# Performance work log

Hardware: AMD Instinct MI355X
Metric: run time of the kernel (lower is better)

Reference implementation:

```python
import jax, jax.numpy as jnp
import numpy as np

B, S, D = 4, 2048, 1024
E, H, TOPK = 8, 4096, 2


def setup_inputs() -> dict:
    key = jax.random.key(0)
    ks = jax.random.split(key, 6)
    scale_d = 1.0 / np.sqrt(D)
    scale_h = 1.0 / np.sqrt(H)
    return {
        "x": jax.random.normal(ks[0], (B, S, D), dtype=jnp.float32),
        "gate_w": jax.random.normal(ks[1], (D, E), dtype=jnp.float32) * scale_d,
        "w1": jax.random.normal(ks[2], (E, D, H), dtype=jnp.float32) * scale_d,
        "b1": jnp.zeros((E, H), dtype=jnp.float32),
        "w2": jax.random.normal(ks[3], (E, H, D), dtype=jnp.float32) * scale_h,
        "b2": jnp.zeros((E, D), dtype=jnp.float32),
    }


def reference(x, gate_w, w1, b1, w2, b2):
    # Gate: logits [B, S, E], top-k routing, softmax over the k selected logits
    gate_logits = jnp.einsum("bsd,de->bse", x, gate_w)
    topw, sel = jax.lax.top_k(gate_logits, TOPK)          # [B, S, K]
    topw = jax.nn.softmax(topw.astype(jnp.float32), axis=-1).astype(x.dtype)

    out = jnp.zeros_like(x)
    # Loop over the small, fixed expert set (structurally distinct params).
    for i in range(E):
        # combine weight for expert i per token (0 if not routed to i)
        coef = jnp.sum(jnp.where(sel == i, topw, jnp.zeros((), x.dtype)), axis=-1)  # [B, S]
        h = jax.nn.gelu(jnp.einsum("bsd,dh->bsh", x, w1[i]) + b1[i])
        y = jnp.einsum("bsh,hd->bsd", h, w2[i]) + b2[i]
        out = out + coef[..., None] * y
    return out
```

## Files before the change

kernel.cpp:

```cpp
#include <hip/hip_runtime.h>
#include <hip/hip_bf16.h>

#define T_TOKENS 8192
#define D_DIM 1024
#define H_DIM 4096
#define E_NUM 8
#define CAP 8192
#define CNT_PAD 16

#define TPB_G 32
#define GATE_BLKS (T_TOKENS / TPB_G)
#define TRW1_BLKS ((D_DIM / 64) * (H_DIM / 64) * E_NUM)
#define TRW2_BLKS ((H_DIM / 64) * (D_DIM / 64) * E_NUM)

typedef short bf16x8 __attribute__((ext_vector_type(8)));
typedef float f32x4 __attribute__((ext_vector_type(4)));
typedef unsigned short u16x8 __attribute__((ext_vector_type(8)));

__device__ inline unsigned short f2bf(float f) {
    __hip_bfloat16 h = __float2bfloat16(f);
    return *reinterpret_cast<unsigned short*>(&h);
}

__device__ inline float gelu_sig(float v) {
    float x = v * (1.5957691216057308f + 0.07135481627f * v * v);
    return v * __builtin_amdgcn_rcpf(1.0f + __expf(-x));
}

__device__ inline void gld_lds16(const unsigned short* g, unsigned short* lds) {
    __builtin_amdgcn_global_load_lds(
        (const __attribute__((address_space(1))) void*)g,
        (__attribute__((address_space(3))) void*)lds, 16, 0, 0);
}

#define WAITV(N) do { asm volatile("s_waitcnt vmcnt(" #N ")" ::: "memory"); \
                      __builtin_amdgcn_sched_barrier(0); } while (0)
#define LGKM0    do { asm volatile("s_waitcnt lgkmcnt(0)" ::: "memory"); \
                      __builtin_amdgcn_sched_barrier(0); } while (0)
#define SBAR     do { __builtin_amdgcn_sched_barrier(0); \
                      __builtin_amdgcn_s_barrier(); \
                      __builtin_amdgcn_sched_barrier(0); } while (0)

#define XCD_ITEMS(T)                                                          \
    int xcd = blockIdx.x & 7;                                                 \
    int lb  = blockIdx.x >> 3;                                                \
    int nbx = gridDim.x >> 3;                                                 \
    int q_ = (T) >> 3, r_ = (T) & 7;                                          \
    int base_ = (xcd < r_) ? xcd * (q_ + 1) : r_ * (q_ + 1) + (xcd - r_) * q_;\
    int cntx_ = (xcd < r_) ? q_ + 1 : q_;

__device__ inline void trw_body(const float* __restrict__ w,
                                unsigned short* __restrict__ wt,
                                int K, int N, int bb,
                                unsigned short (*tb)[72]) {
    int nk = K / 64, nn = N / 64;
    int e = bb / (nk * nn);
    int rem = bb - e * (nk * nn);
    int k0 = (rem % nk) * 64;
    int n0 = (rem / nk) * 64;
    const float* we = w + (size_t)e * K * N + (size_t)k0 * N + n0;
    unsigned short* wte = wt + (size_t)e * K * N + (size_t)n0 * K + k0;
    int tid = threadIdx.x;

    int kg = tid >> 4;
    int nq = (tid & 15) * 4;
    float4 r0 = *(const float4*)(we + (size_t)(kg * 4 + 0) * N + nq);
    float4 r1 = *(const float4*)(we + (size_t)(kg * 4 + 1) * N + nq);
    float4 r2 = *(const float4*)(we + (size_t)(kg * 4 + 2) * N + nq);
    float4 r3 = *(const float4*)(we + (size_t)(kg * 4 + 3) * N + nq);
    ushort4 u;
    u.x = f2bf(r0.x); u.y = f2bf(r1.x); u.z = f2bf(r2.x); u.w = f2bf(r3.x);
    *(ushort4*)&tb[nq + 0][kg * 4] = u;
    u.x = f2bf(r0.y); u.y = f2bf(r1.y); u.z = f2bf(r2.y); u.w = f2bf(r3.y);
    *(ushort4*)&tb[nq + 1][kg * 4] = u;
    u.x = f2bf(r0.z); u.y = f2bf(r1.z); u.z = f2bf(r2.z); u.w = f2bf(r3.z);
    *(ushort4*)&tb[nq + 2][kg * 4] = u;
    u.x = f2bf(r0.w); u.y = f2bf(r1.w); u.z = f2bf(r2.w); u.w = f2bf(r3.w);
    *(ushort4*)&tb[nq + 3][kg * 4] = u;

    __syncthreads();

#pragma unroll
    for (int p = 0; p < 2; ++p) {
        int n = p * 32 + (tid >> 3);
        int kc = (tid & 7) * 8;
        u16x8 v = *(const u16x8*)&tb[n][kc];
        *(u16x8*)(wte + (size_t)n * K + kc) = v;
    }
}

__global__ __launch_bounds__(256) void prep_kernel(const float* __restrict__ x,
                                                   const float* __restrict__ gw,
                                                   const float* __restrict__ w1,
                                                   const float* __restrict__ w2,
                                                   int* __restrict__ cnt,
                                                   int* __restrict__ tok,
                                                   float* __restrict__ cf,
                                                   unsigned short* __restrict__ xb,
                                                   unsigned short* __restrict__ w1t,
                                                   unsigned short* __restrict__ w2t) {
    __shared__ __align__(16) unsigned short tb[64][72];
    __shared__ int ls0[TPB_G], ls1[TPB_G];
    __shared__ float lp0[TPB_G], lp1[TPB_G];
    int b = blockIdx.x;
    if (b >= GATE_BLKS) {
        int bb = b - GATE_BLKS;
        if (bb < TRW1_BLKS) trw_body(w1, w1t, D_DIM, H_DIM, bb, tb);
        else                trw_body(w2, w2t, H_DIM, D_DIM, bb - TRW1_BLKS, tb);
        return;
    }
    int tid = threadIdx.x;
    int lane = tid & 63, wv = tid >> 6;
#pragma unroll
    for (int rep = 0; rep < TPB_G / 4; ++rep) {
        int ti = rep * 4 + wv;
        int t = b * TPB_G + ti;
        const float* xr = x + (size_t)t * D_DIM;
        unsigned short* xbr = xb + (size_t)t * D_DIM;
        double acc[E_NUM];
#pragma unroll
        for (int e = 0; e < E_NUM; ++e) acc[e] = 0.0;
#pragma unroll
        for (int it = 0; it < 4; ++it) {
            int d = it * 256 + lane * 4;
            float4 v = *(const float4*)(xr + d);
            ushort4 u;
            u.x = f2bf(v.x); u.y = f2bf(v.y); u.z = f2bf(v.z); u.w = f2bf(v.w);
            *(ushort4*)(xbr + d) = u;
            const float vv[4] = {v.x, v.y, v.z, v.w};
#pragma unroll
            for (int j = 0; j < 4; ++j) {
                const float* g = gw + (size_t)(d + j) * E_NUM;
#pragma unroll
                for (int e = 0; e < E_NUM; ++e) acc[e] += (double)vv[j] * (double)g[e];
            }
        }
#pragma unroll
        for (int e = 0; e < E_NUM; ++e) {
            double v = acc[e];
#pragma unroll
            for (int off = 32; off >= 1; off >>= 1) v += __shfl_xor(v, off);
            acc[e] = v;
        }
        if (lane == 0) {
            int s0 = 0;
#pragma unroll
            for (int e = 1; e < E_NUM; ++e) if (acc[e] > acc[s0]) s0 = e;
            int s1 = -1;
#pragma unroll
            for (int e = 0; e < E_NUM; ++e) if (e != s0 && (s1 < 0 || acc[e] > acc[s1])) s1 = e;
            float l0 = (float)acc[s0], l1 = (float)acc[s1];
            float p1 = __expf(l1 - l0);
            float inv = 1.0f / (1.0f + p1);
            ls0[ti] = s0; ls1[ti] = s1;
            lp0[ti] = inv; lp1[ti] = p1 * inv;
        }
    }
    __syncthreads();
    if (tid < E_NUM) {
        int e = tid, c = 0;
#pragma unroll
        for (int i = 0; i < TPB_G; ++i) c += (ls0[i] == e) + (ls1[i] == e);
        if (c > 0) {
            int q = atomicAdd(&cnt[e * CNT_PAD], c);
            for (int i = 0; i < TPB_G; ++i) {
                int t = b * TPB_G + i;
                if (ls0[i] == e) { tok[e * CAP + q] = t; cf[e * CAP + q] = lp0[i]; ++q; }
                if (ls1[i] == e) { tok[e * CAP + q] = t; cf[e * CAP + q] = lp1[i]; ++q; }
            }
        }
    }
}


__global__ __launch_bounds__(512, 2) void gemm1_fast(const unsigned short* __restrict__ xb,
                                                     const unsigned short* __restrict__ w1t,
                                                     const float* __restrict__ b1,
                                                     const int* __restrict__ cnt,
                                                     const int* __restrict__ tok,
                                                     unsigned short* __restrict__ Hbuf) {
    __shared__ __align__(16) unsigned short As[3][256][32];
    __shared__ __align__(16) unsigned short Bs[3][256][32];
    __shared__ int s_tok[256];

    int tid = threadIdx.x, lane = tid & 63, wv = tid >> 6;
    int wm = wv >> 2, wn = wv & 3;
    int lm = lane & 15, lkq = lane >> 4;
    int srow = tid >> 2;
    int schunk = (((tid & 3) ^ (srow & 3)) << 3);
    int rdc = ((lkq ^ (lm & 3)) << 3);

    int ne_[E_NUM], offs_[E_NUM], pref[E_NUM + 1];
    pref[0] = 0;
    int off = 0;
#pragma unroll
    for (int e = 0; e < E_NUM; ++e) {
        ne_[e] = cnt[e * CNT_PAD];
        offs_[e] = off; off += ne_[e];
        pref[e + 1] = pref[e] + ((ne_[e] + 255) >> 8) * 16;
    }
    int T = pref[E_NUM];

    XCD_ITEMS(T)
    for (int ii = lb; ii < cntx_; ii += nbx) {
        int w = base_ + ii;
        int e = 0;
#pragma unroll
        for (int q = 0; q < E_NUM - 1; ++q) e += (w >= pref[q + 1]) ? 1 : 0;
        int local = w - pref[e];
        int bm0 = (local >> 4) * 256;
        int n0 = (local & 15) * 256;
        int ne = ne_[e];
        int offs = offs_[e];
        const unsigned short* w1e = w1t + (size_t)e * H_DIM * D_DIM;

        __syncthreads();
        if (tid < 256) s_tok[tid] = tok[e * CAP + min(bm0 + tid, ne - 1)];
        __syncthreads();

        const unsigned short* gA[2];
        const unsigned short* gB[2];
#pragma unroll
        for (int u = 0; u < 2; ++u) {
            gA[u] = xb + (size_t)s_tok[u * 128 + srow] * D_DIM + schunk;
            gB[u] = w1e + (size_t)(n0 + u * 128 + srow) * D_DIM + schunk;
        }
        float bias_v[4];
#pragma unroll
        for (int j = 0; j < 4; ++j)
            bias_v[j] = b1[(size_t)e * H_DIM + n0 + wn * 64 + j * 16 + lm];

        f32x4 acc[8][4];
#pragma unroll
        for (int i = 0; i < 8; ++i)
#pragma unroll
            for (int j = 0; j < 4; ++j) { f32x4 z = {0.f, 0.f, 0.f, 0.f}; acc[i][j] = z; }

        auto STAGE_A = [&](int sl, int kb, int u) {
            gld_lds16(gA[u] + kb * 32, &As[sl][u * 128 + wv * 16][0]);
        };
        auto STAGE_B = [&](int sl, int kb, int u) {
            gld_lds16(gB[u] + kb * 32, &Bs[sl][u * 128 + wv * 16][0]);
        };

        const int NT = D_DIM / 32;
        STAGE_A(0, 0, 0); STAGE_A(0, 0, 1); STAGE_B(0, 0, 0); STAGE_B(0, 0, 1);
        STAGE_A(1, 1, 0); STAGE_A(1, 1, 1); STAGE_B(1, 1, 0); STAGE_B(1, 1, 1);

        int s = 0, s2 = 2;
        for (int t = 0; t < NT; ++t) {
            if (t + 1 < NT) { WAITV(4); } else { WAITV(0); }
            SBAR;
            bf16x8 bfr[4], afr[4];
#pragma unroll
            for (int f = 0; f < 4; ++f)
                bfr[f] = *(const bf16x8*)&Bs[s][wn * 64 + f * 16 + lm][rdc];
#pragma unroll
            for (int f = 0; f < 4; ++f)
                afr[f] = *(const bf16x8*)&As[s][wm * 128 + f * 16 + lm][rdc];
            if (t + 2 < NT) { STAGE_A(s2, t + 2, 0); STAGE_A(s2, t + 2, 1); }
            LGKM0;
            __builtin_amdgcn_s_setprio(1);
#pragma unroll
            for (int i = 0; i < 4; ++i)
#pragma unroll
                for (int j = 0; j < 4; ++j)
                    acc[i][j] = __builtin_amdgcn_mfma_f32_16x16x32_bf16(afr[i], bfr[j], acc[i][j], 0, 0, 0);
            __builtin_amdgcn_s_setprio(0);
#pragma unroll
            for (int f = 0; f < 4; ++f)
                afr[f] = *(const bf16x8*)&As[s][wm * 128 + 64 + f * 16 + lm][rdc];
            if (t + 2 < NT) { STAGE_B(s2, t + 2, 0); STAGE_B(s2, t + 2, 1); }
            LGKM0;
            __builtin_amdgcn_s_setprio(1);
#pragma unroll
            for (int i = 0; i < 4; ++i)
#pragma unroll
                for (int j = 0; j < 4; ++j)
                    acc[4 + i][j] = __builtin_amdgcn_mfma_f32_16x16x32_bf16(afr[i], bfr[j], acc[4 + i][j], 0, 0, 0);
            __builtin_amdgcn_s_setprio(0);
            s = (s == 2) ? 0 : s + 1;
            s2 = (s2 == 2) ? 0 : s2 + 1;
        }

#pragma unroll
        for (int i = 0; i < 8; ++i) {
            int frow = wm * 128 + ((i < 4) ? i * 16 : 64 + (i - 4) * 16);
#pragma unroll
            for (int r = 0; r < 4; ++r) {
                int row = frow + lkq * 4 + r;
                int gr = bm0 + row;
                if (gr >= ne) continue;
                size_t rb = (size_t)(offs + gr) * H_DIM;
#pragma unroll
                for (int j = 0; j < 4; ++j) {
                    int gn = n0 + wn * 64 + j * 16 + lm;
                    float v = acc[i][j][r] + bias_v[j];
                    Hbuf[rb + gn] = f2bf(gelu_sig(v));
                }
            }
        }
    }
}

__global__ __launch_bounds__(512, 2) void gemm2_fast(const unsigned short* __restrict__ Hbuf,
                                                     const unsigned short* __restrict__ w2t,
                                                     const float* __restrict__ b2,
                                                     const int* __restrict__ cnt,
                                                     const int* __restrict__ tok,
                                                     const float* __restrict__ cf,
                                                     float* __restrict__ out) {
    __shared__ __align__(16) unsigned short As[3][256][32];
    __shared__ __align__(16) unsigned short Bs[3][256][32];
    __shared__ int s_tok[256];
    __shared__ float s_cf[256];

    int tid = threadIdx.x, lane = tid & 63, wv = tid >> 6;
    int wm = wv >> 2, wn = wv & 3;
    int lm = lane & 15, lkq = lane >> 4;
    int srow = tid >> 2;
    int schunk = (((tid & 3) ^ (srow & 3)) << 3);
    int rdc = ((lkq ^ (lm & 3)) << 3);

    int ne_[E_NUM], offs_[E_NUM], pref[E_NUM + 1];
    pref[0] = 0;
    int off = 0;
#pragma unroll
    for (int e = 0; e < E_NUM; ++e) {
        ne_[e] = cnt[e * CNT_PAD];
        offs_[e] = off; off += ne_[e];
        pref[e + 1] = pref[e] + ((ne_[e] + 255) >> 8) * 4;
    }
    int T = pref[E_NUM];

    XCD_ITEMS(T)
    for (int ii = lb; ii < cntx_; ii += nbx) {
        int w = base_ + ii;
        int e = 0;
#pragma unroll
        for (int q = 0; q < E_NUM - 1; ++q) e += (w >= pref[q + 1]) ? 1 : 0;
        int local = w - pref[e];
        int bm0 = (local >> 2) * 256;
        int n0 = (local & 3) * 256;
        int ne = ne_[e];
        int offs = offs_[e];
        const unsigned short* w2e = w2t + (size_t)e * H_DIM * D_DIM;

        __syncthreads();
        if (tid < 256) {
            int gi = min(bm0 + tid, ne - 1);
            s_tok[tid] = tok[e * CAP + gi];
            s_cf[tid] = cf[e * CAP + gi];
        }
        __syncthreads();

        const unsigned short* gA[2];
        const unsigned short* gB[2];
#pragma unroll
        for (int u = 0; u < 2; ++u) {
            gA[u] = Hbuf + (size_t)(offs + min(bm0 + u * 128 + srow, ne - 1)) * H_DIM + schunk;
            gB[u] = w2e + (size_t)(n0 + u * 128 + srow) * H_DIM + schunk;
        }
        float bias_v[4];
#pragma unroll
        for (int j = 0; j < 4; ++j)
            bias_v[j] = b2[(size_t)e * D_DIM + n0 + wn * 64 + j * 16 + lm];

        f32x4 acc[8][4];
#pragma unroll
        for (int i = 0; i < 8; ++i)
#pragma unroll
            for (int j = 0; j < 4; ++j) { f32x4 z = {0.f, 0.f, 0.f, 0.f}; acc[i][j] = z; }

        auto STAGE_A = [&](int sl, int kb, int u) {
            gld_lds16(gA[u] + kb * 32, &As[sl][u * 128 + wv * 16][0]);
        };
        auto STAGE_B = [&](int sl, int kb, int u) {
            gld_lds16(gB[u] + kb * 32, &Bs[sl][u * 128 + wv * 16][0]);
        };

        const int NT = H_DIM / 32;
        STAGE_A(0, 0, 0); STAGE_A(0, 0, 1); STAGE_B(0, 0, 0); STAGE_B(0, 0, 1);
        STAGE_A(1, 1, 0); STAGE_A(1, 1, 1); STAGE_B(1, 1, 0); STAGE_B(1, 1, 1);

        int s = 0, s2 = 2;
        for (int t = 0; t < NT; ++t) {
            if (t + 1 < NT) { WAITV(4); } else { WAITV(0); }
            SBAR;
            bf16x8 bfr[4], afr[4];
#pragma unroll
            for (int f = 0; f < 4; ++f)
                bfr[f] = *(const bf16x8*)&Bs[s][wn * 64 + f * 16 + lm][rdc];
#pragma unroll
            for (int f = 0; f < 4; ++f)
                afr[f] = *(const bf16x8*)&As[s][wm * 128 + f * 16 + lm][rdc];
            if (t + 2 < NT) { STAGE_A(s2, t + 2, 0); STAGE_A(s2, t + 2, 1); }
            LGKM0;
            __builtin_amdgcn_s_setprio(1);
#pragma unroll
            for (int i = 0; i < 4; ++i)
#pragma unroll
                for (int j = 0; j < 4; ++j)
                    acc[i][j] = __builtin_amdgcn_mfma_f32_16x16x32_bf16(afr[i], bfr[j], acc[i][j], 0, 0, 0);
            __builtin_amdgcn_s_setprio(0);
#pragma unroll
            for (int f = 0; f < 4; ++f)
                afr[f] = *(const bf16x8*)&As[s][wm * 128 + 64 + f * 16 + lm][rdc];
            if (t + 2 < NT) { STAGE_B(s2, t + 2, 0); STAGE_B(s2, t + 2, 1); }
            LGKM0;
            __builtin_amdgcn_s_setprio(1);
#pragma unroll
            for (int i = 0; i < 4; ++i)
#pragma unroll
                for (int j = 0; j < 4; ++j)
                    acc[4 + i][j] = __builtin_amdgcn_mfma_f32_16x16x32_bf16(afr[i], bfr[j], acc[4 + i][j], 0, 0, 0);
            __builtin_amdgcn_s_setprio(0);
            s = (s == 2) ? 0 : s + 1;
            s2 = (s2 == 2) ? 0 : s2 + 1;
        }

#pragma unroll
        for (int i = 0; i < 8; ++i) {
            int frow = wm * 128 + ((i < 4) ? i * 16 : 64 + (i - 4) * 16);
#pragma unroll
            for (int r = 0; r < 4; ++r) {
                int row = frow + lkq * 4 + r;
                int gr = bm0 + row;
                if (gr >= ne) continue;
                int tk = s_tok[row];
                float cw = s_cf[row];
#pragma unroll
                for (int j = 0; j < 4; ++j) {
                    int gn = n0 + wn * 64 + j * 16 + lm;
                    float y = acc[i][j][r] + bias_v[j];
                    atomicAdd(&out[(size_t)tk * D_DIM + gn], cw * y);
                }
            }
        }
    }
}

extern "C" void kernel_launch(void* const* d_in, const int* in_sizes, int n_in,
                              void* d_out, int out_size, void* d_ws, size_t ws_size,
                              hipStream_t stream) {
    const float* x  = (const float*)d_in[0];
    const float* gw = (const float*)d_in[1];
    const float* w1 = (const float*)d_in[2];
    const float* b1 = (const float*)d_in[3];
    const float* w2 = (const float*)d_in[4];
    const float* b2 = (const float*)d_in[5];
    float* out = (float*)d_out;

    char* ws = (char*)d_ws;
    const size_t SZ_CNT   = E_NUM * CNT_PAD * 4;
    const size_t SZ_ROUTE = SZ_CNT + (size_t)2 * E_NUM * CAP * 4;
    const size_t SZ_XB    = (size_t)T_TOKENS * D_DIM * 2;
    const size_t SZ_W     = (size_t)E_NUM * D_DIM * H_DIM * 2;
    const size_t SZ_H     = (size_t)2 * T_TOKENS * H_DIM * 2;

    int*   cnt = (int*)ws;
    int*   tok = (int*)(ws + SZ_CNT);
    float* cff = (float*)(ws + SZ_CNT + E_NUM * CAP * 4);

    size_t need_fast = SZ_ROUTE + SZ_XB + 2 * SZ_W + SZ_H;
    if (ws_size < need_fast) return;

    unsigned short* xb   = (unsigned short*)(ws + SZ_ROUTE);
    unsigned short* w1t  = (unsigned short*)(ws + SZ_ROUTE + SZ_XB);
    unsigned short* w2t  = (unsigned short*)(ws + SZ_ROUTE + SZ_XB + SZ_W);
    unsigned short* Hbuf = (unsigned short*)(ws + SZ_ROUTE + SZ_XB + 2 * SZ_W);

    hipMemsetAsync(cnt, 0, SZ_CNT, stream);
    hipMemsetAsync(out, 0, (size_t)out_size * sizeof(float), stream);

    prep_kernel<<<GATE_BLKS + TRW1_BLKS + TRW2_BLKS, 256, 0, stream>>>(
        x, gw, w1, w2, cnt, tok, cff, xb, w1t, w2t);

    gemm1_fast<<<256, 512, 0, stream>>>(xb, w1t, b1, cnt, tok, Hbuf);
    gemm2_fast<<<256, 512, 0, stream>>>(Hbuf, w2t, b2, cnt, tok, cff, out);
}
```

Baseline: 614.1 us.

## Restructure MoE GEMM mainloops to BK=64 ping-pong with quarter-step staging

Both expert GEMM kernels move from a three-stage BK=32 LDS ring to two BK=64 ping-pong buffers. Each K step is split into four quadrant phases that interleave fragment loads, async global-to-LDS staging of the next tile, and MFMA bursts, separated by barriers. The XOR swizzle widens to 8 chunks and launch bounds drop to one block per CU to fit the larger LDS footprint. The aim is fewer barriers per unit of MFMA work and better load/compute overlap, at the cost of occupancy and more barriers inside each step.

```diff
diff --git a/kernel.cpp b/kernel.cpp
--- a/kernel.cpp
+++ b/kernel.cpp
@@ -33,13 +33,13 @@
         (__attribute__((address_space(3))) void*)lds, 16, 0, 0);
 }
 
-#define WAITV(N) do { asm volatile("s_waitcnt vmcnt(" #N ")" ::: "memory"); \
-                      __builtin_amdgcn_sched_barrier(0); } while (0)
-#define LGKM0    do { asm volatile("s_waitcnt lgkmcnt(0)" ::: "memory"); \
-                      __builtin_amdgcn_sched_barrier(0); } while (0)
-#define SBAR     do { __builtin_amdgcn_sched_barrier(0); \
-                      __builtin_amdgcn_s_barrier(); \
-                      __builtin_amdgcn_sched_barrier(0); } while (0)
+#define WAITV0 do { asm volatile("s_waitcnt vmcnt(0)" ::: "memory"); \
+                    __builtin_amdgcn_sched_barrier(0); } while (0)
+#define LGKM0  do { asm volatile("s_waitcnt lgkmcnt(0)" ::: "memory"); \
+                    __builtin_amdgcn_sched_barrier(0); } while (0)
+#define SBAR   do { __builtin_amdgcn_sched_barrier(0); \
+                    __builtin_amdgcn_s_barrier(); \
+                    __builtin_amdgcn_sched_barrier(0); } while (0)
 
 #define XCD_ITEMS(T)                                                          \
     int xcd = blockIdx.x & 7;                                                 \
@@ -173,22 +173,45 @@
 }
 
 
-__global__ __launch_bounds__(512, 2) void gemm1_fast(const unsigned short* __restrict__ xb,
+#define GEMM_CORE(AR, BR, AW, BW, tcur, last)                                 \
+    WAITV0; SBAR;                                                             \
+                                                     \
+    LDA4(AR, 0); LDB2(BR, 0);                                                 \
+    if (!(last)) { STG_A(AW, (tcur) + 1, 0); STG_B(BW, (tcur) + 1, 0); }      \
+    LGKM0; MMQ(0, 0);                                                         \
+    SBAR;                                                                     \
+                                                     \
+    LDB2(BR, 1);                                                              \
+    if (!(last)) { STG_A(AW, (tcur) + 1, 1); STG_B(BW, (tcur) + 1, 1); }      \
+    LGKM0; MMQ(0, 1);                                                         \
+    SBAR;                                                                     \
+                                     \
+    LDA4(AR, 1);                                                              \
+    if (!(last)) { STG_A(AW, (tcur) + 1, 2); STG_B(BW, (tcur) + 1, 2); }      \
+    LGKM0; MMQ(1, 1);                                                         \
+    SBAR;                                                                     \
+                                                     \
+    LDB2(BR, 0);                                                              \
+    if (!(last)) { STG_A(AW, (tcur) + 1, 3); STG_B(BW, (tcur) + 1, 3); }      \
+    LGKM0; MMQ(1, 0);
+
+__global__ __launch_bounds__(512, 1) void gemm1_fast(const unsigned short* __restrict__ xb,
                                                      const unsigned short* __restrict__ w1t,
                                                      const float* __restrict__ b1,
                                                      const int* __restrict__ cnt,
                                                      const int* __restrict__ tok,
                                                      unsigned short* __restrict__ Hbuf) {
-    __shared__ __align__(16) unsigned short As[3][256][32];
-    __shared__ __align__(16) unsigned short Bs[3][256][32];
+    __shared__ __align__(16) unsigned short As0[256][64], Bs0[256][64];
+    __shared__ __align__(16) unsigned short As1[256][64], Bs1[256][64];
     __shared__ int s_tok[256];
 
     int tid = threadIdx.x, lane = tid & 63, wv = tid >> 6;
     int wm = wv >> 2, wn = wv & 3;
     int lm = lane & 15, lkq = lane >> 4;
-    int srow = tid >> 2;
-    int schunk = (((tid & 3) ^ (srow & 3)) << 3);
-    int rdc = ((lkq ^ (lm & 3)) << 3);
+    int srow = tid >> 3;
+    int schunk = ((tid & 7) ^ (srow & 7)) << 3;
+    int rdc0 = ((lkq ^ (lm & 7)) << 3);
+    int rdc1 = (((4 + lkq) ^ (lm & 7)) << 3);
 
     int ne_[E_NUM], offs_[E_NUM], pref[E_NUM + 1];
     pref[0] = 0;
@@ -218,13 +241,12 @@
         if (tid < 256) s_tok[tid] = tok[e * CAP + min(bm0 + tid, ne - 1)];
         __syncthreads();
 
-        const unsigned short* gA[2];
-        const unsigned short* gB[2];
-#pragma unroll
-        for (int u = 0; u < 2; ++u) {
-            gA[u] = xb + (size_t)s_tok[u * 128 + srow] * D_DIM + schunk;
-            gB[u] = w1e + (size_t)(n0 + u * 128 + srow) * D_DIM + schunk;
-        }
+        const unsigned short* gA[4];
+#pragma unroll
+        for (int q = 0; q < 4; ++q)
+            gA[q] = xb + (size_t)s_tok[q * 64 + srow] * D_DIM + schunk;
+        const unsigned short* gB = w1e + (size_t)(n0 + srow) * D_DIM + schunk;
+
         float bias_v[4];
 #pragma unroll
         for (int j = 0; j < 4; ++j)
@@ -236,59 +258,59 @@
 #pragma unroll
             for (int j = 0; j < 4; ++j) { f32x4 z = {0.f, 0.f, 0.f, 0.f}; acc[i][j] = z; }
 
-        auto STAGE_A = [&](int sl, int kb, int u) {
-            gld_lds16(gA[u] + kb * 32, &As[sl][u * 128 + wv * 16][0]);
+        bf16x8 afr[4][2], bfr[2][2];
+
+        auto STG_A = [&](unsigned short (&A)[256][64], int kb, int q) {
+            gld_lds16(gA[q] + kb * 64, &A[q * 64 + wv * 8][0]);
         };
-        auto STAGE_B = [&](int sl, int kb, int u) {
-            gld_lds16(gB[u] + kb * 32, &Bs[sl][u * 128 + wv * 16][0]);
+        auto STG_B = [&](unsigned short (&B)[256][64], int kb, int q) {
+            gld_lds16(gB + (size_t)(q * 64) * D_DIM + kb * 64, &B[q * 64 + wv * 8][0]);
         };
-
-        const int NT = D_DIM / 32;
-        STAGE_A(0, 0, 0); STAGE_A(0, 0, 1); STAGE_B(0, 0, 0); STAGE_B(0, 0, 1);
-        STAGE_A(1, 1, 0); STAGE_A(1, 1, 1); STAGE_B(1, 1, 0); STAGE_B(1, 1, 1);
-
-        int s = 0, s2 = 2;
-        for (int t = 0; t < NT; ++t) {
-            if (t + 1 < NT) { WAITV(4); } else { WAITV(0); }
-            SBAR;
-            bf16x8 bfr[4], afr[4];
-#pragma unroll
-            for (int f = 0; f < 4; ++f)
-                bfr[f] = *(const bf16x8*)&Bs[s][wn * 64 + f * 16 + lm][rdc];
-#pragma unroll
-            for (int f = 0; f < 4; ++f)
-                afr[f] = *(const bf16x8*)&As[s][wm * 128 + f * 16 + lm][rdc];
-            if (t + 2 < NT) { STAGE_A(s2, t + 2, 0); STAGE_A(s2, t + 2, 1); }
-            LGKM0;
-            __builtin_amdgcn_s_setprio(1);
-#pragma unroll
-            for (int i = 0; i < 4; ++i)
-#pragma unroll
-                for (int j = 0; j < 4; ++j)
-                    acc[i][j] = __builtin_amdgcn_mfma_f32_16x16x32_bf16(afr[i], bfr[j], acc[i][j], 0, 0, 0);
-            __builtin_amdgcn_s_setprio(0);
-#pragma unroll
-            for (int f = 0; f < 4; ++f)
-                afr[f] = *(const bf16x8*)&As[s][wm * 128 + 64 + f * 16 + lm][rdc];
-            if (t + 2 < NT) { STAGE_B(s2, t + 2, 0); STAGE_B(s2, t + 2, 1); }
-            LGKM0;
-            __builtin_amdgcn_s_setprio(1);
-#pragma unroll
-            for (int i = 0; i < 4; ++i)
-#pragma unroll
-                for (int j = 0; j < 4; ++j)
-                    acc[4 + i][j] = __builtin_amdgcn_mfma_f32_16x16x32_bf16(afr[i], bfr[j], acc[4 + i][j], 0, 0, 0);
-            __builtin_amdgcn_s_setprio(0);
-            s = (s == 2) ? 0 : s + 1;
-            s2 = (s2 == 2) ? 0 : s2 + 1;
-        }
+#define LDA4(AR, mh)                                                          \
+        _Pragma("unroll")                                                     \
+        for (int f = 0; f < 4; ++f) {                                         \
+            int row = wm * 128 + ((mh) * 4 + f) * 16 + lm;                    \
+            afr[f][0] = *(const bf16x8*)&AR[row][rdc0];                       \
+            afr[f][1] = *(const bf16x8*)&AR[row][rdc1];                       \
+        }
+#define LDB2(BR, nh)                                                          \
+        _Pragma("unroll")                                                     \
+        for (int j = 0; j < 2; ++j) {                                         \
+            int col = wn * 64 + ((nh) * 2 + j) * 16 + lm;                     \
+            bfr[j][0] = *(const bf16x8*)&BR[col][rdc0];                       \
+            bfr[j][1] = *(const bf16x8*)&BR[col][rdc1];                       \
+        }
+#define MMQ(mh, nh)                                                           \
+        __builtin_amdgcn_s_setprio(1);                                        \
+        _Pragma("unroll")                                                     \
+        for (int f = 0; f < 4; ++f)                                           \
+            _Pragma("unroll")                                                 \
+            for (int j = 0; j < 2; ++j) {                                     \
+                acc[(mh) * 4 + f][(nh) * 2 + j] =                             \
+                    __builtin_amdgcn_mfma_f32_16x16x32_bf16(                  \
+                        afr[f][0], bfr[j][0], acc[(mh) * 4 + f][(nh) * 2 + j], 0, 0, 0); \
+                acc[(mh) * 4 + f][(nh) * 2 + j] =                             \
+                    __builtin_amdgcn_mfma_f32_16x16x32_bf16(                  \
+                        afr[f][1], bfr[j][1], acc[(mh) * 4 + f][(nh) * 2 + j], 0, 0, 0); \
+            }                                                                 \
+        __builtin_amdgcn_s_setprio(0);
+
+        const int NT = D_DIM / 64;
+#pragma unroll
+        for (int q = 0; q < 4; ++q) { STG_A(As0, 0, q); STG_B(Bs0, 0, q); }
+        for (int t = 0; t < NT; t += 2) {
+            GEMM_CORE(As0, Bs0, As1, Bs1, t, false)
+            GEMM_CORE(As1, Bs1, As0, Bs0, t + 1, (t + 2 >= NT))
+        }
+#undef LDA4
+#undef LDB2
+#undef MMQ
 
 #pragma unroll
         for (int i = 0; i < 8; ++i) {
-            int frow = wm * 128 + ((i < 4) ? i * 16 : 64 + (i - 4) * 16);
 #pragma unroll
             for (int r = 0; r < 4; ++r) {
-                int row = frow + lkq * 4 + r;
+                int row = wm * 128 + i * 16 + lkq * 4 + r;
                 int gr = bm0 + row;
                 if (gr >= ne) continue;
                 size_t rb = (size_t)(offs + gr) * H_DIM;
@@ -303,24 +325,25 @@
     }
 }
 
-__global__ __launch_bounds__(512, 2) void gemm2_fast(const unsigned short* __restrict__ Hbuf,
+__global__ __launch_bounds__(512, 1) void gemm2_fast(const unsigned short* __restrict__ Hbuf,
                                                      const unsigned short* __restrict__ w2t,
                                                      const float* __restrict__ b2,
                                                      const int* __restrict__ cnt,
                                                      const int* __restrict__ tok,
                                                      const float* __restrict__ cf,
                                                      float* __restrict__ out) {
-    __shared__ __align__(16) unsigned short As[3][256][32];
-    __shared__ __align__(16) unsigned short Bs[3][256][32];
+    __shared__ __align__(16) unsigned short As0[256][64], Bs0[256][64];
+    __shared__ __align__(16) unsigned short As1[256][64], Bs1[256][64];
     __shared__ int s_tok[256];
     __shared__ float s_cf[256];
 
     int tid = threadIdx.x, lane = tid & 63, wv = tid >> 6;
     int wm = wv >> 2, wn = wv & 3;
     int lm = lane & 15, lkq = lane >> 4;
-    int srow = tid >> 2;
-    int schunk = (((tid & 3) ^ (srow & 3)) << 3);
-    int rdc = ((lkq ^ (lm & 3)) << 3);
+    int srow = tid >> 3;
+    int schunk = ((tid & 7) ^ (srow & 7)) << 3;
+    int rdc0 = ((lkq ^ (lm & 7)) << 3);
+    int rdc1 = (((4 + lkq) ^ (lm & 7)) << 3);
 
     int ne_[E_NUM], offs_[E_NUM], pref[E_NUM + 1];
     pref[0] = 0;
@@ -354,13 +377,12 @@
         }
         __syncthreads();
 
-        const unsigned short* gA[2];
-        const unsigned short* gB[2];
-#pragma unroll
-        for (int u = 0; u < 2; ++u) {
-            gA[u] = Hbuf + (size_t)(offs + min(bm0 + u * 128 + srow, ne - 1)) * H_DIM + schunk;
-            gB[u] = w2e + (size_t)(n0 + u * 128 + srow) * H_DIM + schunk;
-        }
+        const unsigned short* gA[4];
+#pragma unroll
+        for (int q = 0; q < 4; ++q)
+            gA[q] = Hbuf + (size_t)(offs + min(bm0 + q * 64 + srow, ne - 1)) * H_DIM + schunk;
+        const unsigned short* gB = w2e + (size_t)(n0 + srow) * H_DIM + schunk;
+
         float bias_v[4];
 #pragma unroll
         for (int j = 0; j < 4; ++j)
@@ -372,59 +394,59 @@
 #pragma unroll
             for (int j = 0; j < 4; ++j) { f32x4 z = {0.f, 0.f, 0.f, 0.f}; acc[i][j] = z; }
 
-        auto STAGE_A = [&](int sl, int kb, int u) {
-            gld_lds16(gA[u] + kb * 32, &As[sl][u * 128 + wv * 16][0]);
+        bf16x8 afr[4][2], bfr[2][2];
+
+        auto STG_A = [&](unsigned short (&A)[256][64], int kb, int q) {
+            gld_lds16(gA[q] + kb * 64, &A[q * 64 + wv * 8][0]);
         };
-        auto STAGE_B = [&](int sl, int kb, int u) {
-            gld_lds16(gB[u] + kb * 32, &Bs[sl][u * 128 + wv * 16][0]);
+        auto STG_B = [&](unsigned short (&B)[256][64], int kb, int q) {
+            gld_lds16(gB + (size_t)(q * 64) * H_DIM + kb * 64, &B[q * 64 + wv * 8][0]);
         };
-
-        const int NT = H_DIM / 32;
-        STAGE_A(0, 0, 0); STAGE_A(0, 0, 1); STAGE_B(0, 0, 0); STAGE_B(0, 0, 1);
-        STAGE_A(1, 1, 0); STAGE_A(1, 1, 1); STAGE_B(1, 1, 0); STAGE_B(1, 1, 1);
-
-        int s = 0, s2 = 2;
-        for (int t = 0; t < NT; ++t) {
-            if (t + 1 < NT) { WAITV(4); } else { WAITV(0); }
-            SBAR;
-            bf16x8 bfr[4], afr[4];
-#pragma unroll
-            for (int f = 0; f < 4; ++f)
-                bfr[f] = *(const bf16x8*)&Bs[s][wn * 64 + f * 16 + lm][rdc];
-#pragma unroll
-            for (int f = 0; f < 4; ++f)
-                afr[f] = *(const bf16x8*)&As[s][wm * 128 + f * 16 + lm][rdc];
-            if (t + 2 < NT) { STAGE_A(s2, t + 2, 0); STAGE_A(s2, t + 2, 1); }
-            LGKM0;
-            __builtin_amdgcn_s_setprio(1);
-#pragma unroll
-            for (int i = 0; i < 4; ++i)
-#pragma unroll
-                for (int j = 0; j < 4; ++j)
-                    acc[i][j] = __builtin_amdgcn_mfma_f32_16x16x32_bf16(afr[i], bfr[j], acc[i][j], 0, 0, 0);
-            __builtin_amdgcn_s_setprio(0);
-#pragma unroll
-            for (int f = 0; f < 4; ++f)
-                afr[f] = *(const bf16x8*)&As[s][wm * 128 + 64 + f * 16 + lm][rdc];
-            if (t + 2 < NT) { STAGE_B(s2, t + 2, 0); STAGE_B(s2, t + 2, 1); }
-            LGKM0;
-            __builtin_amdgcn_s_setprio(1);
-#pragma unroll
-            for (int i = 0; i < 4; ++i)
-#pragma unroll
-                for (int j = 0; j < 4; ++j)
-                    acc[4 + i][j] = __builtin_amdgcn_mfma_f32_16x16x32_bf16(afr[i], bfr[j], acc[4 + i][j], 0, 0, 0);
-            __builtin_amdgcn_s_setprio(0);
-            s = (s == 2) ? 0 : s + 1;
-            s2 = (s2 == 2) ? 0 : s2 + 1;
-        }
+#define LDA4(AR, mh)                                                          \
+        _Pragma("unroll")                                                     \
+        for (int f = 0; f < 4; ++f) {                                         \
+            int row = wm * 128 + ((mh) * 4 + f) * 16 + lm;                    \
+            afr[f][0] = *(const bf16x8*)&AR[row][rdc0];                       \
+            afr[f][1] = *(const bf16x8*)&AR[row][rdc1];                       \
+        }
+#define LDB2(BR, nh)                                                          \
+        _Pragma("unroll")                                                     \
+        for (int j = 0; j < 2; ++j) {                                         \
+            int col = wn * 64 + ((nh) * 2 + j) * 16 + lm;                     \
+            bfr[j][0] = *(const bf16x8*)&BR[col][rdc0];                       \
+            bfr[j][1] = *(const bf16x8*)&BR[col][rdc1];                       \
+        }
+#define MMQ(mh, nh)                                                           \
+        __builtin_amdgcn_s_setprio(1);                                        \
+        _Pragma("unroll")                                                     \
+        for (int f = 0; f < 4; ++f)                                           \
+            _Pragma("unroll")                                                 \
+            for (int j = 0; j < 2; ++j) {                                     \
+                acc[(mh) * 4 + f][(nh) * 2 + j] =                             \
+                    __builtin_amdgcn_mfma_f32_16x16x32_bf16(                  \
+                        afr[f][0], bfr[j][0], acc[(mh) * 4 + f][(nh) * 2 + j], 0, 0, 0); \
+                acc[(mh) * 4 + f][(nh) * 2 + j] =                             \
+                    __builtin_amdgcn_mfma_f32_16x16x32_bf16(                  \
+                        afr[f][1], bfr[j][1], acc[(mh) * 4 + f][(nh) * 2 + j], 0, 0, 0); \
+            }                                                                 \
+        __builtin_amdgcn_s_setprio(0);
+
+        const int NT = H_DIM / 64;
+#pragma unroll
+        for (int q = 0; q < 4; ++q) { STG_A(As0, 0, q); STG_B(Bs0, 0, q); }
+        for (int t = 0; t < NT; t += 2) {
+            GEMM_CORE(As0, Bs0, As1, Bs1, t, false)
+            GEMM_CORE(As1, Bs1, As0, Bs0, t + 1, (t + 2 >= NT))
+        }
+#undef LDA4
+#undef LDB2
+#undef MMQ
 
 #pragma unroll
         for (int i = 0; i < 8; ++i) {
-            int frow = wm * 128 + ((i < 4) ? i * 16 : 64 + (i - 4) * 16);
 #pragma unroll
             for (int r = 0; r < 4; ++r) {
-                int row = frow + lkq * 4 + r;
+                int row = wm * 128 + i * 16 + lkq * 4 + r;
                 int gr = bm0 + row;
                 if (gr >= ne) continue;
                 int tk = s_tok[row];
```

New measurement: 620.5 us. About the same (+1.0%).
